# Performance work log

Measured on AMD Instinct MI355X. Metric: run time of the kernel, lower is better.

## Reference

```python
import jax, jax.numpy as jnp
import numpy as np

HEADS = 16


def setup_inputs() -> dict:
    key = jax.random.key(0)
    ks = jax.random.split(key, 5)
    n, s, d = 2, 2048, 1024
    return {
        "x": jax.random.normal(ks[0], (n, s, d), dtype=jnp.float32),
        "Wqkv": jax.random.normal(ks[1], (3 * d, d), dtype=jnp.float32) * (d ** -0.5),
        "bqkv": jax.random.normal(ks[2], (3 * d,), dtype=jnp.float32) * 0.02,
        "Wd": jax.random.normal(ks[3], (d, d), dtype=jnp.float32) * (d ** -0.5),
        "bd": jax.random.normal(ks[4], (d,), dtype=jnp.float32) * 0.02,
        "mask": 1,
    }


def reference(x, Wqkv, bqkv, Wd, bd, mask):
    n, s, d = x.shape
    h = HEADS
    hd = d // h
    qkv = x @ Wqkv.T + bqkv  # [n, s, 3d]
    q, k, v = jnp.split(qkv, 3, axis=-1)
    # [n, h, s, hd]
    q = q.reshape(n, s, h, hd).transpose(0, 2, 1, 3)
    k = k.reshape(n, s, h, hd).transpose(0, 2, 1, 3)
    v = v.reshape(n, s, h, hd).transpose(0, 2, 1, 3)
    scores = jnp.einsum("bhqd,bhkd->bhqk", q, k)
    if mask:
        causal = jnp.triu(jnp.ones((s, s), dtype=bool), k=1)
        scores = jnp.where(causal, -jnp.inf, scores)
    attn = jax.nn.softmax(scores / jnp.sqrt(jnp.float32(hd)), axis=-1)
    out = jnp.einsum("bhqk,bhkd->bhqd", attn, v)
    out = out.transpose(0, 2, 1, 3).reshape(n, s, d)
    return out @ Wd.T + bd
```

## Files before the change

### kernel.cpp

```cpp
#include <hip/hip_runtime.h>
#include <hip/hip_bf16.h>
#include <cstdint>
#include <cstddef>

typedef __attribute__((ext_vector_type(8))) short bf8_t;
typedef __attribute__((ext_vector_type(4))) float f4_t;

__device__ __forceinline__ unsigned short f2bf(float f) {
    union { float f; unsigned int u; } v; v.f = f;
    unsigned int u = v.u + 0x7FFFu + ((v.u >> 16) & 1u);
    return (unsigned short)(u >> 16);
}

__device__ __forceinline__ void gl_lds16(const void* g, void* l) {
    __builtin_amdgcn_global_load_lds(
        (const __attribute__((address_space(1))) unsigned int*)g,
        (__attribute__((address_space(3))) unsigned int*)l,
        16, 0, 0);
}

__global__ void cvt_kernel(const float* __restrict__ x,    unsigned short* __restrict__ xb,
                           const float* __restrict__ wq,   unsigned short* __restrict__ wqb,
                           const float* __restrict__ wd,   unsigned short* __restrict__ wdb) {
    int i = blockIdx.x * blockDim.x + threadIdx.x;
    const float* src; unsigned short* dst; int off;
    if (i < 1048576)       { src = x;  dst = xb;  off = i; }
    else if (i < 1835008)  { src = wq; dst = wqb; off = i - 1048576; }
    else                   { src = wd; dst = wdb; off = i - 1835008; }
    float4 f = ((const float4*)src)[off];
    ushort4 o;
    o.x = f2bf(f.x); o.y = f2bf(f.y); o.z = f2bf(f.z); o.w = f2bf(f.w);
    ((ushort4*)dst)[off] = o;
}

template<int MODE, int TM>
__global__ __launch_bounds__(256, 2) void gemm_bt_kernel(
    const unsigned short* __restrict__ A,
    const unsigned short* __restrict__ W,
    const float* __restrict__ bias,
    float* __restrict__ outf,
    unsigned short* __restrict__ qb,
    unsigned short* __restrict__ kb,
    unsigned short* __restrict__ vtb,
    int K, int Nn)
{
    constexpr int HM = TM / 2;
    constexpr int MB = HM / 16;
    constexpr int AI = TM / 32;

    __shared__ unsigned short As[TM][64];
    __shared__ unsigned short Bs[128][64];

    const int tid  = threadIdx.x;
    const int lane = tid & 63;
    const int w    = tid >> 6;
    const int wm   = w & 1;
    const int wn   = w >> 1;
    const int quad = lane >> 4;
    const int l16  = lane & 15;
    const int m0   = blockIdx.y * TM;
    const int n0   = blockIdx.x * 128;

    const int lrow = lane >> 3;
    const int lcol = ((lane & 7) ^ lrow) << 3;

    f4_t acc[MB][4];
    {
        f4_t z = {0.f, 0.f, 0.f, 0.f};
        #pragma unroll
        for (int i = 0; i < MB; ++i)
            #pragma unroll
            for (int j = 0; j < 4; ++j) acc[i][j] = z;
    }

    const unsigned short* Agp = A + (size_t)(m0 + w * (TM / 4) + lrow) * K + lcol;
    const unsigned short* Bgp = W + (size_t)(n0 + w * 32 + lrow) * K + lcol;
    unsigned short* lAp = &As[w * (TM / 4)][0];
    unsigned short* lBp = &Bs[w * 32][0];

    for (int kk = 0; kk < K; kk += 64) {
        __syncthreads();
        #pragma unroll
        for (int i = 0; i < AI; ++i)
            gl_lds16(Agp + (size_t)(i * 8) * K + kk, lAp + i * 8 * 64);
        #pragma unroll
        for (int i = 0; i < 4; ++i)
            gl_lds16(Bgp + (size_t)(i * 8) * K + kk, lBp + i * 8 * 64);
        __syncthreads();

        const int sw = l16 & 7;
        #pragma unroll
        for (int ks = 0; ks < 2; ++ks) {
            bf8_t af[MB], bfr[4];
            #pragma unroll
            for (int mb = 0; mb < MB; ++mb)
                af[mb] = *(const bf8_t*)&As[wm * HM + mb * 16 + l16][(((ks << 2) | quad) ^ sw) << 3];
            #pragma unroll
            for (int nb = 0; nb < 4; ++nb)
                bfr[nb] = *(const bf8_t*)&Bs[wn * 64 + nb * 16 + l16][(((ks << 2) | quad) ^ sw) << 3];
            #pragma unroll
            for (int mb = 0; mb < MB; ++mb)
                #pragma unroll
                for (int nb = 0; nb < 4; ++nb)
                    acc[mb][nb] = __builtin_amdgcn_mfma_f32_16x16x32_bf16(af[mb], bfr[nb], acc[mb][nb], 0, 0, 0);
        }
    }

    #pragma unroll
    for (int nb = 0; nb < 4; ++nb) {
        const int col = n0 + wn * 64 + nb * 16 + l16;
        const float bc = bias[col];
        const int which  = col >> 10;
        const int within = col & 1023;
        const int head   = within >> 6;
        const int hdi    = within & 63;
        #pragma unroll
        for (int mb = 0; mb < MB; ++mb) {
            #pragma unroll
            for (int r = 0; r < 4; ++r) {
                const int row = m0 + wm * HM + mb * 16 + quad * 4 + r;
                const float v = acc[mb][nb][r] + bc;
                if (MODE == 0) {
                    const int b  = row >> 11;
                    const int sq = row & 2047;
                    const int bh = b * 16 + head;
                    const unsigned short bv = f2bf(v);
                    if (which == 0)      qb [((size_t)bh * 2048 + sq) * 64 + hdi] = bv;
                    else if (which == 1) kb [((size_t)bh * 2048 + sq) * 64 + hdi] = bv;
                    else                 vtb[((size_t)bh * 64 + hdi) * 2048 + sq] = bv;
                } else {
                    outf[(size_t)row * Nn + col] = v;
                }
            }
        }
    }
}

__global__ __launch_bounds__(256, 2) void attn_kernel(
    const unsigned short* __restrict__ qg,
    const unsigned short* __restrict__ kg,
    const unsigned short* __restrict__ vg,
    unsigned short* __restrict__ ao)
{
    __shared__ unsigned short QP[64][72];
    __shared__ unsigned short Ks[2][64][72];
    __shared__ unsigned short Vs[2][64][72];

    const int tid  = threadIdx.x;
    const int lane = tid & 63;
    const int w    = tid >> 6;
    const int quad = lane >> 4;
    const int l16  = lane & 15;
    const int bx   = blockIdx.x;
    const int bh   = ((bx & 7) << 2) + ((bx >> 3) & 3);
    const int jj   = bx >> 5;
    const int qtBig   = 31 - jj;
    const int qtSmall = jj;
    const int b    = bh >> 4;
    const int head = bh & 15;

    const unsigned short* Qp = qg + (size_t)bh * 2048 * 64;
    const unsigned short* Kp = kg + (size_t)bh * 2048 * 64;
    const unsigned short* Vp = vg + (size_t)bh * 64 * 2048;

    const int sr = tid >> 2;
    const int sc = (tid & 3) << 4;

    float4 q0a = *(const float4*)(Qp + (size_t)(qtBig * 64 + sr) * 64 + sc);
    float4 q0b = *(const float4*)(Qp + (size_t)(qtBig * 64 + sr) * 64 + sc + 8);
    float4 q1a = *(const float4*)(Qp + (size_t)(qtSmall * 64 + sr) * 64 + sc);
    float4 q1b = *(const float4*)(Qp + (size_t)(qtSmall * 64 + sr) * 64 + sc + 8);

    float4 k0 = *(const float4*)(Kp + (size_t)sr * 64 + sc);
    float4 k1 = *(const float4*)(Kp + (size_t)sr * 64 + sc + 8);
    float4 v0 = *(const float4*)(Vp + (size_t)sr * 2048 + sc);
    float4 v1 = *(const float4*)(Vp + (size_t)sr * 2048 + sc + 8);

    *(float4*)&QP[sr][sc]     = q0a;
    *(float4*)&QP[sr][sc + 8] = q0b;
    bf8_t aq[2];
    aq[0] = *(const bf8_t*)&QP[w * 16 + l16][quad * 8];
    aq[1] = *(const bf8_t*)&QP[w * 16 + l16][32 + quad * 8];

    bf8_t bones;
    {
        const short one = (l16 == 0) ? (short)0x3F80 : (short)0;
        #pragma unroll
        for (int j = 0; j < 8; ++j) bones[j] = one;
    }

    f4_t oacc[4];
    f4_t lacc;
    {
        f4_t z = {0.f, 0.f, 0.f, 0.f};
        #pragma unroll
        for (int j = 0; j < 4; ++j) oacc[j] = z;
        lacc = z;
    }

    auto epilogue = [&](int qt) {
        #pragma unroll
        for (int r = 0; r < 4; ++r) {
            const float lsum = __shfl(lacc[r], lane & 48);
            const float rl = 1.f / lsum;
            const int sq = qt * 64 + (w << 4) + (quad << 2) + r;
            #pragma unroll
            for (int nb = 0; nb < 4; ++nb) {
                const int dcol = head * 64 + nb * 16 + l16;
                ao[((size_t)(b * 2048 + sq)) * 1024 + dcol] = f2bf(oacc[nb][r] * rl);
            }
        }
    };

    const int p0len = 32 - jj;

    for (int t = 0; t < 33; ++t) {
        const int buf = t & 1;
        *(float4*)&Ks[buf][sr][sc]     = k0;
        *(float4*)&Ks[buf][sr][sc + 8] = k1;
        *(float4*)&Vs[buf][sr][sc]     = v0;
        *(float4*)&Vs[buf][sr][sc + 8] = v1;
        __syncthreads();

        if (t + 1 < 33) {
            const int t2 = t + 1;
            const size_t sk = (size_t)((t2 >= p0len) ? (t2 - p0len) : t2) << 6;
            k0 = *(const float4*)(Kp + (sk + sr) * 64 + sc);
            k1 = *(const float4*)(Kp + (sk + sr) * 64 + sc + 8);
            v0 = *(const float4*)(Vp + (size_t)sr * 2048 + sk + sc);
            v1 = *(const float4*)(Vp + (size_t)sr * 2048 + sk + sc + 8);
        }

        if (t == p0len) {
            epilogue(qtBig);
            f4_t z = {0.f, 0.f, 0.f, 0.f};
            #pragma unroll
            for (int j = 0; j < 4; ++j) oacc[j] = z;
            lacc = z;
            *(float4*)&QP[sr][sc]     = q1a;
            *(float4*)&QP[sr][sc + 8] = q1b;
            aq[0] = *(const bf8_t*)&QP[w * 16 + l16][quad * 8];
            aq[1] = *(const bf8_t*)&QP[w * 16 + l16][32 + quad * 8];
        }

        const bool ph1 = (t >= p0len);
        const int  kt  = ph1 ? (t - p0len) : t;
        const int  qt  = ph1 ? qtSmall : qtBig;
        const bool diag = (kt == qt);

        f4_t sacc[4];
        {
            f4_t z = {0.f, 0.f, 0.f, 0.f};
            #pragma unroll
            for (int j = 0; j < 4; ++j) sacc[j] = z;
        }
        #pragma unroll
        for (int ks = 0; ks < 2; ++ks) {
            #pragma unroll
            for (int nb = 0; nb < 4; ++nb) {
                bf8_t bk = *(const bf8_t*)&Ks[buf][nb * 16 + l16][ks * 32 + quad * 8];
                sacc[nb] = __builtin_amdgcn_mfma_f32_16x16x32_bf16(aq[ks], bk, sacc[nb], 0, 0, 0);
            }
        }

        #pragma unroll
        for (int r = 0; r < 4; ++r) {
            const int rloc = (w << 4) + (quad << 2) + r;
            #pragma unroll
            for (int nb = 0; nb < 4; ++nb) {
                float e = fmaf(sacc[nb][r], 0.18033688f, -20.197731f);
                if (diag && (nb * 16 + l16 > rloc)) e = -1e30f;
                union { float f; unsigned int u; } pv;
                pv.f = exp2f(e);
                QP[rloc][nb * 16 + l16] = (unsigned short)(pv.u >> 16);
            }
        }

        #pragma unroll
        for (int ks = 0; ks < 2; ++ks) {
            bf8_t ap = *(const bf8_t*)&QP[(w << 4) + l16][ks * 32 + quad * 8];
            #pragma unroll
            for (int nb = 0; nb < 4; ++nb) {
                bf8_t bv = *(const bf8_t*)&Vs[buf][nb * 16 + l16][ks * 32 + quad * 8];
                oacc[nb] = __builtin_amdgcn_mfma_f32_16x16x32_bf16(ap, bv, oacc[nb], 0, 0, 0);
            }
            lacc = __builtin_amdgcn_mfma_f32_16x16x32_bf16(ap, bones, lacc, 0, 0, 0);
        }
    }

    epilogue(qtSmall);
}

extern "C" void kernel_launch(void* const* d_in, const int* in_sizes, int n_in,
                              void* d_out, int out_size, void* d_ws, size_t ws_size,
                              hipStream_t stream) {
    const float* x    = (const float*)d_in[0];
    const float* Wqkv = (const float*)d_in[1];
    const float* bqkv = (const float*)d_in[2];
    const float* Wd   = (const float*)d_in[3];
    const float* bd   = (const float*)d_in[4];
    float* out = (float*)d_out;

    char* ws = (char*)d_ws;
    unsigned short* xb    = (unsigned short*)(ws);
    unsigned short* wqkvb = (unsigned short*)(ws + 8388608);
    unsigned short* wdb   = (unsigned short*)(ws + 14680064);
    unsigned short* qb2   = (unsigned short*)(ws + 16777216);
    unsigned short* kb2   = (unsigned short*)(ws + 25165824);
    unsigned short* vtb   = (unsigned short*)(ws + 33554432);
    unsigned short* ao    = xb;

    cvt_kernel<<<8192, 256, 0, stream>>>(x, xb, Wqkv, wqkvb, Wd, wdb);

    gemm_bt_kernel<0, 128><<<dim3(24, 32), 256, 0, stream>>>(
        xb, wqkvb, bqkv, nullptr, qb2, kb2, vtb, 1024, 3072);

    attn_kernel<<<512, 256, 0, stream>>>(qb2, kb2, vtb, ao);

    gemm_bt_kernel<1, 64><<<dim3(8, 64), 256, 0, stream>>>(
        ao, wdb, bd, out, nullptr, nullptr, nullptr, 1024, 1024);
}
```

Measured before the change: 183.4 us.

## Split attention KV loop across two blocks with partial merge and swizzled LDS

```diff
diff --git a/kernel.cpp b/kernel.cpp
--- a/kernel.cpp
+++ b/kernel.cpp
@@ -10,6 +10,10 @@
     union { float f; unsigned int u; } v; v.f = f;
     unsigned int u = v.u + 0x7FFFu + ((v.u >> 16) & 1u);
     return (unsigned short)(u >> 16);
+}
+__device__ __forceinline__ float bf2f(unsigned short s) {
+    union { unsigned int u; float f; } v; v.u = ((unsigned int)s) << 16;
+    return v.f;
 }
 
 __device__ __forceinline__ void gl_lds16(const void* g, void* l) {
@@ -136,15 +140,17 @@
     }
 }
 
-__global__ __launch_bounds__(256, 2) void attn_kernel(
+__global__ __launch_bounds__(256, 4) void attn_kernel(
     const unsigned short* __restrict__ qg,
     const unsigned short* __restrict__ kg,
     const unsigned short* __restrict__ vg,
-    unsigned short* __restrict__ ao)
+    unsigned short* __restrict__ ao,
+    unsigned short* __restrict__ pO,
+    float* __restrict__ pL)
 {
-    __shared__ unsigned short QP[64][72];
-    __shared__ unsigned short Ks[2][64][72];
-    __shared__ unsigned short Vs[2][64][72];
+    __shared__ unsigned short Ks[2][4096];
+    __shared__ unsigned short Vs[2][4096];
+    __shared__ unsigned short Ps[4096];
 
     const int tid  = threadIdx.x;
     const int lane = tid & 63;
@@ -152,35 +158,34 @@
     const int quad = lane >> 4;
     const int l16  = lane & 15;
     const int bx   = blockIdx.x;
-    const int bh   = ((bx & 7) << 2) + ((bx >> 3) & 3);
-    const int jj   = bx >> 5;
+    const int bh   = ((bx & 7) << 2) | ((bx >> 3) & 3);
+    const int h    = (bx >> 5) & 1;
+    const int jj   = bx >> 6;
     const int qtBig   = 31 - jj;
     const int qtSmall = jj;
     const int b    = bh >> 4;
     const int head = bh & 15;
+    const int p0len = 32 - jj;
+    const int t0 = h ? 17 : 0;
+    const int t1 = h ? 33 : 17;
 
     const unsigned short* Qp = qg + (size_t)bh * 2048 * 64;
     const unsigned short* Kp = kg + (size_t)bh * 2048 * 64;
     const unsigned short* Vp = vg + (size_t)bh * 64 * 2048;
 
-    const int sr = tid >> 2;
-    const int sc = (tid & 3) << 4;
-
-    float4 q0a = *(const float4*)(Qp + (size_t)(qtBig * 64 + sr) * 64 + sc);
-    float4 q0b = *(const float4*)(Qp + (size_t)(qtBig * 64 + sr) * 64 + sc + 8);
-    float4 q1a = *(const float4*)(Qp + (size_t)(qtSmall * 64 + sr) * 64 + sc);
-    float4 q1b = *(const float4*)(Qp + (size_t)(qtSmall * 64 + sr) * 64 + sc + 8);
-
-    float4 k0 = *(const float4*)(Kp + (size_t)sr * 64 + sc);
-    float4 k1 = *(const float4*)(Kp + (size_t)sr * 64 + sc + 8);
-    float4 v0 = *(const float4*)(Vp + (size_t)sr * 2048 + sc);
-    float4 v1 = *(const float4*)(Vp + (size_t)sr * 2048 + sc + 8);
-
-    *(float4*)&QP[sr][sc]     = q0a;
-    *(float4*)&QP[sr][sc + 8] = q0b;
-    bf8_t aq[2];
-    aq[0] = *(const bf8_t*)&QP[w * 16 + l16][quad * 8];
-    aq[1] = *(const bf8_t*)&QP[w * 16 + l16][32 + quad * 8];
+    const int srow = lane >> 3;
+    const int scol = ((lane & 7) ^ srow) << 3;
+    const unsigned short* kga = Kp + (size_t)(w * 16 + srow) * 64 + scol;
+    const unsigned short* vga = Vp + (size_t)(w * 16 + srow) * 2048 + scol;
+    const int sw = l16 & 7;
+
+    auto stageKV = [&](int kt, int buf) {
+        const int sk0 = kt << 6;
+        gl_lds16(kga + (size_t)sk0 * 64,       &Ks[buf][w * 16 * 64]);
+        gl_lds16(kga + (size_t)sk0 * 64 + 512, &Ks[buf][(w * 16 + 8) * 64]);
+        gl_lds16(vga + sk0,                    &Vs[buf][w * 16 * 64]);
+        gl_lds16(vga + sk0 + 8 * 2048,         &Vs[buf][(w * 16 + 8) * 64]);
+    };
 
     bf8_t bones;
     {
@@ -198,55 +203,56 @@
         lacc = z;
     }
 
-    auto epilogue = [&](int qt) {
+    bf8_t aq[2];
+    {
+        const int qt_init = (t0 >= p0len) ? qtSmall : qtBig;
+        const size_t qrow = (size_t)(qt_init * 64 + w * 16 + l16) * 64;
+        aq[0] = *(const bf8_t*)(Qp + qrow + quad * 8);
+        aq[1] = *(const bf8_t*)(Qp + qrow + 32 + quad * 8);
+    }
+
+    auto flushPartial = [&]() {
+        const int tb = (h << 9) + (bh << 4) + jj;
+        unsigned short* po = pO + (size_t)tb * 4096;
         #pragma unroll
         for (int r = 0; r < 4; ++r) {
-            const float lsum = __shfl(lacc[r], lane & 48);
-            const float rl = 1.f / lsum;
-            const int sq = qt * 64 + (w << 4) + (quad << 2) + r;
-            #pragma unroll
-            for (int nb = 0; nb < 4; ++nb) {
-                const int dcol = head * 64 + nb * 16 + l16;
-                ao[((size_t)(b * 2048 + sq)) * 1024 + dcol] = f2bf(oacc[nb][r] * rl);
-            }
+            const int row = w * 16 + quad * 4 + r;
+            #pragma unroll
+            for (int nb = 0; nb < 4; ++nb)
+                po[row * 64 + nb * 16 + l16] = f2bf(oacc[nb][r]);
+            if (l16 == 0) pL[tb * 64 + row] = lacc[r];
         }
     };
 
-    const int p0len = 32 - jj;
-
-    for (int t = 0; t < 33; ++t) {
+    {
+        const int kt0 = (t0 >= p0len) ? (t0 - p0len) : t0;
+        stageKV(kt0, t0 & 1);
+    }
+
+    for (int t = t0; t < t1; ++t) {
         const int buf = t & 1;
-        *(float4*)&Ks[buf][sr][sc]     = k0;
-        *(float4*)&Ks[buf][sr][sc + 8] = k1;
-        *(float4*)&Vs[buf][sr][sc]     = v0;
-        *(float4*)&Vs[buf][sr][sc + 8] = v1;
         __syncthreads();
 
-        if (t + 1 < 33) {
+        if (t + 1 < t1) {
             const int t2 = t + 1;
-            const size_t sk = (size_t)((t2 >= p0len) ? (t2 - p0len) : t2) << 6;
-            k0 = *(const float4*)(Kp + (sk + sr) * 64 + sc);
-            k1 = *(const float4*)(Kp + (sk + sr) * 64 + sc + 8);
-            v0 = *(const float4*)(Vp + (size_t)sr * 2048 + sk + sc);
-            v1 = *(const float4*)(Vp + (size_t)sr * 2048 + sk + sc + 8);
+            stageKV((t2 >= p0len) ? (t2 - p0len) : t2, t2 & 1);
         }
 
         if (t == p0len) {
-            epilogue(qtBig);
+            flushPartial();
             f4_t z = {0.f, 0.f, 0.f, 0.f};
             #pragma unroll
             for (int j = 0; j < 4; ++j) oacc[j] = z;
             lacc = z;
-            *(float4*)&QP[sr][sc]     = q1a;
-            *(float4*)&QP[sr][sc + 8] = q1b;
-            aq[0] = *(const bf8_t*)&QP[w * 16 + l16][quad * 8];
-            aq[1] = *(const bf8_t*)&QP[w * 16 + l16][32 + quad * 8];
+            const size_t qrow = (size_t)(qtSmall * 64 + w * 16 + l16) * 64;
+            aq[0] = *(const bf8_t*)(Qp + qrow + quad * 8);
+            aq[1] = *(const bf8_t*)(Qp + qrow + 32 + quad * 8);
         }
 
         const bool ph1 = (t >= p0len);
         const int  kt  = ph1 ? (t - p0len) : t;
-        const int  qt  = ph1 ? qtSmall : qtBig;
-        const bool diag = (kt == qt);
+        const int  qtc = ph1 ? qtSmall : qtBig;
+        const bool diag = (kt == qtc);
 
         f4_t sacc[4];
         {
@@ -258,7 +264,7 @@
         for (int ks = 0; ks < 2; ++ks) {
             #pragma unroll
             for (int nb = 0; nb < 4; ++nb) {
-                bf8_t bk = *(const bf8_t*)&Ks[buf][nb * 16 + l16][ks * 32 + quad * 8];
+                bf8_t bk = *(const bf8_t*)&Ks[buf][(nb * 16 + l16) * 64 + (((((ks << 2) | quad)) ^ sw) << 3)];
                 sacc[nb] = __builtin_amdgcn_mfma_f32_16x16x32_bf16(aq[ks], bk, sacc[nb], 0, 0, 0);
             }
         }
@@ -266,29 +272,67 @@
         #pragma unroll
         for (int r = 0; r < 4; ++r) {
             const int rloc = (w << 4) + (quad << 2) + r;
+            const int rk = rloc & 7;
             #pragma unroll
             for (int nb = 0; nb < 4; ++nb) {
                 float e = fmaf(sacc[nb][r], 0.18033688f, -20.197731f);
                 if (diag && (nb * 16 + l16 > rloc)) e = -1e30f;
                 union { float f; unsigned int u; } pv;
                 pv.f = exp2f(e);
-                QP[rloc][nb * 16 + l16] = (unsigned short)(pv.u >> 16);
+                Ps[rloc * 64 + ((((nb << 1) | (l16 >> 3)) ^ rk) << 3) + (l16 & 7)] =
+                    (unsigned short)(pv.u >> 16);
             }
         }
 
         #pragma unroll
         for (int ks = 0; ks < 2; ++ks) {
-            bf8_t ap = *(const bf8_t*)&QP[(w << 4) + l16][ks * 32 + quad * 8];
+            bf8_t ap = *(const bf8_t*)&Ps[(w * 16 + l16) * 64 + ((((ks << 2) | quad) ^ sw) << 3)];
             #pragma unroll
             for (int nb = 0; nb < 4; ++nb) {
-                bf8_t bv = *(const bf8_t*)&Vs[buf][nb * 16 + l16][ks * 32 + quad * 8];
+                bf8_t bv = *(const bf8_t*)&Vs[buf][(nb * 16 + l16) * 64 + ((((ks << 2) | quad) ^ sw) << 3)];
                 oacc[nb] = __builtin_amdgcn_mfma_f32_16x16x32_bf16(ap, bv, oacc[nb], 0, 0, 0);
             }
             lacc = __builtin_amdgcn_mfma_f32_16x16x32_bf16(ap, bones, lacc, 0, 0, 0);
         }
     }
 
-    epilogue(qtSmall);
+    if (!h) {
+        flushPartial();
+    } else {
+        #pragma unroll
+        for (int r = 0; r < 4; ++r) {
+            const float lsum = __shfl(lacc[r], lane & 48);
+            const float rl = 1.f / lsum;
+            const int sq = qtSmall * 64 + (w << 4) + (quad << 2) + r;
+            #pragma unroll
+            for (int nb = 0; nb < 4; ++nb) {
+                const int dcol = head * 64 + nb * 16 + l16;
+                ao[((size_t)(b * 2048 + sq)) * 1024 + dcol] = f2bf(oacc[nb][r] * rl);
+            }
+        }
+    }
+}
+
+__global__ void merge_kernel(const unsigned short* __restrict__ pO,
+                             const float* __restrict__ pL,
+                             unsigned short* __restrict__ ao) {
+    const int blk  = blockIdx.x;
+    const int bh   = blk >> 4;
+    const int jj   = blk & 15;
+    const int b    = bh >> 4;
+    const int head = bh & 15;
+    const int qt   = 31 - jj;
+    const int row  = threadIdx.x >> 2;
+    const int c0   = (threadIdx.x & 3) << 4;
+
+    const float l = pL[blk * 64 + row] + pL[(512 + blk) * 64 + row];
+    const float rl = 1.f / l;
+    const unsigned short* p0 = pO + (size_t)blk * 4096 + row * 64 + c0;
+    const unsigned short* p1 = pO + (size_t)(512 + blk) * 4096 + row * 64 + c0;
+    unsigned short* dst = ao + ((size_t)(b * 2048 + qt * 64 + row)) * 1024 + head * 64 + c0;
+    #pragma unroll
+    for (int j = 0; j < 16; ++j)
+        dst[j] = f2bf((bf2f(p0[j]) + bf2f(p1[j])) * rl);
 }
 
 extern "C" void kernel_launch(void* const* d_in, const int* in_sizes, int n_in,
@@ -308,6 +352,8 @@
     unsigned short* qb2   = (unsigned short*)(ws + 16777216);
     unsigned short* kb2   = (unsigned short*)(ws + 25165824);
     unsigned short* vtb   = (unsigned short*)(ws + 33554432);
+    unsigned short* pO    = (unsigned short*)(ws + 41943040);
+    float*          pL    = (float*)(ws + 50331648);
     unsigned short* ao    = xb;
 
     cvt_kernel<<<8192, 256, 0, stream>>>(x, xb, Wqkv, wqkvb, Wd, wdb);
@@ -315,7 +361,9 @@
     gemm_bt_kernel<0, 128><<<dim3(24, 32), 256, 0, stream>>>(
         xb, wqkvb, bqkv, nullptr, qb2, kb2, vtb, 1024, 3072);
 
-    attn_kernel<<<512, 256, 0, stream>>>(qb2, kb2, vtb, ao);
+    attn_kernel<<<1024, 256, 0, stream>>>(qb2, kb2, vtb, ao, pO, pL);
+
+    merge_kernel<<<512, 256, 0, stream>>>(pO, pL, ao);
 
     gemm_bt_kernel<1, 64><<<dim3(8, 64), 256, 0, stream>>>(
         ao, wdb, bd, out, nullptr, nullptr, nullptr, 1024, 1024);
```

Measured after the change: 180.7 us. About the same (-1.5%).
